# Performance work log

Measured on AMD Instinct MI355X. Metric: run time of the kernel, lower is better.

## Reference

```python
import jax, jax.numpy as jnp
import numpy as np

NUM_CLASSES = 10000
FEAT_DIM = 1024
BATCH = 4096


def setup_inputs() -> dict:
    key = jax.random.key(0)
    k1, k2 = jax.random.split(key)
    feat = jax.random.normal(k1, (BATCH, FEAT_DIM), dtype=jnp.float32)
    centers = jax.random.normal(k2, (NUM_CLASSES, FEAT_DIM), dtype=jnp.float32)
    return {"feat": feat, "centers": centers}


def reference(feat, centers):
    # logits = -0.5 * ||feat_b - center_c||^2, computed via the GEMM rewrite
    # ||a-b||^2 = ||a||^2 + ||b||^2 - 2 a.b  (same math as broadcast-sub-square-sum,
    # but avoids the [B, C, D] intermediate and uses tensor-core matmul).
    feat_sq = jnp.sum(feat * feat, axis=-1, keepdims=True)          # [B, 1]
    cent_sq = jnp.sum(centers * centers, axis=-1)[None, :]          # [1, C]
    cross = jnp.einsum('bd,cd->bc', feat, centers)                  # [B, C]
    dist = feat_sq + cent_sq - 2.0 * cross                          # [B, C]
    logits = -0.5 * dist
    return logits
```

## Files before the change

### kernel.cpp

```cpp
#include <hip/hip_runtime.h>
#include <hip/hip_bf16.h>
#include <stdint.h>

#define M_DIM 4096
#define N_DIM 10000
#define K_DIM 1024
#define GM (M_DIM / 256)
#define GN ((N_DIM + 255) / 256)
#define NT (K_DIM / 32)

typedef __attribute__((ext_vector_type(8))) short bf16x8;
typedef __attribute__((ext_vector_type(4))) float f32x4;

#define BAR()      asm volatile("s_barrier" ::: "memory")
#define WAITVM4()  asm volatile("s_waitcnt vmcnt(4)" ::: "memory")
#define WAITVM0()  asm volatile("s_waitcnt vmcnt(0)" ::: "memory")
#define WAITLGKM() asm volatile("s_waitcnt lgkmcnt(0)" ::: "memory")

__device__ __forceinline__ void async_ld16(const void* g, void* l) {
    __builtin_amdgcn_global_load_lds(
        (const __attribute__((address_space(1))) unsigned int*)g,
        (__attribute__((address_space(3))) unsigned int*)l,
        16, 0, 0);
}

__device__ __forceinline__ unsigned short f2bf(float f) {
    unsigned u = __float_as_uint(f);
    unsigned r = (u + 0x7FFFu + ((u >> 16) & 1u)) >> 16;
    return (unsigned short)r;
}

__global__ __launch_bounds__(256) void prep_rows(
    const float* __restrict__ feat, const float* __restrict__ cent,
    unsigned short* __restrict__ featbf, unsigned short* __restrict__ centbf,
    float* __restrict__ fsq, float* __restrict__ csq)
{
    const int wlane = threadIdx.x & 63;
    const int wid   = blockIdx.x * 4 + (threadIdx.x >> 6);
    const int nw    = gridDim.x * 4;
    for (int row = wid; row < M_DIM + N_DIM; row += nw) {
        const float* in;
        unsigned short* outb;
        float* sqp;
        if (row < M_DIM) {
            in = feat + (size_t)row * K_DIM;
            outb = featbf + (size_t)row * K_DIM;
            sqp = fsq + row;
        } else {
            const int r2 = row - M_DIM;
            in = cent + (size_t)r2 * K_DIM;
            outb = centbf + (size_t)r2 * K_DIM;
            sqp = csq + r2;
        }
        float s = 0.f;
        #pragma unroll
        for (int c = 0; c < 4; c++) {
            float4 v = ((const float4*)in)[wlane + c * 64];
            ushort4 pk;
            pk.x = f2bf(v.x); pk.y = f2bf(v.y); pk.z = f2bf(v.z); pk.w = f2bf(v.w);
            ((ushort4*)outb)[wlane + c * 64] = pk;
            s += v.x * v.x + v.y * v.y + v.z * v.z + v.w * v.w;
        }
        #pragma unroll
        for (int off = 32; off > 0; off >>= 1) s += __shfl_down(s, off, 64);
        if (wlane == 0) *sqp = s;
    }
}

__global__ __launch_bounds__(512, 2) void gemm_bt(
    const unsigned short* __restrict__ A,
    const unsigned short* __restrict__ B,
    const float* __restrict__ fsq, const float* __restrict__ csq,
    float* __restrict__ out)
{
    __shared__ unsigned short smem[49152];

    const int tid  = threadIdx.x;
    const int lane = tid & 63;
    const int wave = tid >> 6;
    const int wm = wave & 1;
    const int wn = wave >> 1;
    const int mlane = lane & 15;
    const int quad  = lane >> 4;
    const int fr  = (mlane >> 1) & 3;
    const int qx  = (quad ^ fr) << 4;

    const int bid = blockIdx.x;
    const int xcd = bid & 7;
    const int idx = bid >> 3;
    const int r0  = xcd * 80 + idx;
    const int bm  = r0 & 15;
    const int bn  = r0 >> 4;

    const int arow_base = bm * 256;
    const int brow_base = bn * 256;

    const unsigned short* gA[2];
    const unsigned short* gB[2];
    int ldsA[2], ldsB[2];
    #pragma unroll
    for (int i = 0; i < 2; i++) {
        const int s   = i * 512 + tid;
        const int row = s >> 2;
        const int sc  = s & 3;
        const int kof = (sc ^ ((row >> 1) & 3)) << 3;
        gA[i] = A + (size_t)(arow_base + row) * K_DIM + kof;
        int br = brow_base + row; if (br > N_DIM - 1) br = N_DIM - 1;
        gB[i] = B + (size_t)br * K_DIM + kof;
        ldsA[i] = s * 16;
        ldsB[i] = 16384 + s * 16;
    }

    #define STAGE_A(t2, nbb)                                                  \
        do {                                                                  \
            async_ld16(gA[0] + (size_t)(t2) * 32, (char*)smem + (nbb) + ldsA[0]); \
            async_ld16(gA[1] + (size_t)(t2) * 32, (char*)smem + (nbb) + ldsA[1]); \
        } while (0)
    #define STAGE_B(t2, nbb)                                                  \
        do {                                                                  \
            async_ld16(gB[0] + (size_t)(t2) * 32, (char*)smem + (nbb) + ldsB[0]); \
            async_ld16(gB[1] + (size_t)(t2) * 32, (char*)smem + (nbb) + ldsB[1]); \
        } while (0)

    f32x4 acc[8][4];
    #pragma unroll
    for (int i = 0; i < 8; i++)
        #pragma unroll
        for (int j = 0; j < 4; j++) {
            f32x4 z = {0.f, 0.f, 0.f, 0.f};
            acc[i][j] = z;
        }

    const int aBase = (wm * 128 + mlane) * 64 + qx;
    const int bBase = 16384 + (wn * 64 + mlane) * 64 + qx;

    STAGE_A(0, 0); STAGE_B(0, 0);
    STAGE_A(1, 32768); STAGE_B(1, 32768);
    WAITVM4();
    BAR();

    int bb = 0;
    for (int t = 0; t < NT; ++t) {
        int nb = bb - 32768; if (nb < 0) nb = 65536;
        const char* base = (const char*)smem + bb;
        bf16x8 af[4], bfv[4];

        #pragma unroll
        for (int i = 0; i < 4; i++) {
            af[i]  = *(const bf16x8*)(base + aBase + i * 1024);
            bfv[i] = *(const bf16x8*)(base + bBase + i * 1024);
        }
        if (t + 2 < NT) STAGE_A(t + 2, nb);
        BAR();
        WAITLGKM();
        __builtin_amdgcn_s_setprio(1);
        #pragma unroll
        for (int i = 0; i < 4; i++)
            #pragma unroll
            for (int j = 0; j < 4; j++)
                acc[i][j] = __builtin_amdgcn_mfma_f32_16x16x32_bf16(
                    af[i], bfv[j], acc[i][j], 0, 0, 0);
        __builtin_amdgcn_s_setprio(0);
        BAR();

        #pragma unroll
        for (int i = 0; i < 4; i++)
            af[i] = *(const bf16x8*)(base + aBase + 4096 + i * 1024);
        if (t + 2 < NT) STAGE_B(t + 2, nb);
        BAR();
        WAITLGKM();
        __builtin_amdgcn_s_setprio(1);
        #pragma unroll
        for (int i = 0; i < 4; i++)
            #pragma unroll
            for (int j = 0; j < 4; j++)
                acc[4 + i][j] = __builtin_amdgcn_mfma_f32_16x16x32_bf16(
                    af[i], bfv[j], acc[4 + i][j], 0, 0, 0);
        __builtin_amdgcn_s_setprio(0);

        if (t < NT - 1) {
            if (t + 2 < NT) { WAITVM4(); } else { WAITVM0(); }
        }
        BAR();

        bb += 32768; if (bb > 65536) bb = 0;
    }
    #undef STAGE_A
    #undef STAGE_B

    float* W = (float*)smem + wave * 1088;
    const int rbase0 = arow_base + wm * 128;
    const int cbase  = brow_base + wn * 64 + mlane;
    const int rb_col4 = mlane * 4;
    const int gcol4  = brow_base + wn * 64 + rb_col4;
    const bool colok = gcol4 < N_DIM;

    #pragma unroll
    for (int i = 0; i < 8; i++) {
        float frow[4];
        #pragma unroll
        for (int r = 0; r < 4; r++)
            frow[r] = -0.5f * fsq[rbase0 + i * 16 + quad * 4 + r];
        #pragma unroll
        for (int j = 0; j < 4; j++) {
            int col = cbase + j * 16;
            float cs = -0.5f * csq[col < N_DIM ? col : (N_DIM - 1)];
            #pragma unroll
            for (int r = 0; r < 4; r++)
                W[(quad * 4 + r) * 68 + j * 16 + mlane] = acc[i][j][r] + frow[r] + cs;
        }
        WAITLGKM();
        #pragma unroll
        for (int s = 0; s < 4; s++) {
            int rl = s * 4 + quad;
            f32x4 v = *(const f32x4*)&W[rl * 68 + rb_col4];
            if (colok) {
                int grow = rbase0 + i * 16 + rl;
                __builtin_nontemporal_store(v, (f32x4*)&out[(size_t)grow * N_DIM + gcol4]);
            }
        }
        WAITLGKM();
    }
}

extern "C" void kernel_launch(void* const* d_in, const int* in_sizes, int n_in,
                              void* d_out, int out_size, void* d_ws, size_t ws_size,
                              hipStream_t stream) {
    const float* feat = (const float*)d_in[0];
    const float* cent = (const float*)d_in[1];
    float* out = (float*)d_out;

    char* ws = (char*)d_ws;
    unsigned short* featbf = (unsigned short*)ws;
    unsigned short* centbf = (unsigned short*)(ws + 8388608);
    float* fsq = (float*)(ws + 8388608 + 20480000);
    float* csq = (float*)(ws + 8388608 + 20480000 + 16384);

    prep_rows<<<1024, 256, 0, stream>>>(feat, cent, featbf, centbf, fsq, csq);

    gemm_bt<<<GM * GN, 512, 0, stream>>>(featbf, centbf, fsq, csq, out);
}
```

Before: 293.1 us.

## Deepen GEMM pipeline to four LDS stages and split K-step into quarter phases

Grows shared memory from three to four 32KB buffers so global-to-LDS prefetch runs three K-tiles ahead instead of two. Each K iteration is split into four phases that each read two A fragments and issue one async load, with a barrier between phases. This aims to hide more global-load latency and interleave loads with MFMA more finely. In exchange it uses 128KB LDS per block, which may cut the number of blocks per CU below the two that launch_bounds requests, and it adds more barriers per iteration.

Result: no change. 295.5 us (+0.8%).

```diff
diff --git a/kernel.cpp b/kernel.cpp
--- a/kernel.cpp
+++ b/kernel.cpp
@@ -13,6 +13,7 @@
 typedef __attribute__((ext_vector_type(4))) float f32x4;
 
 #define BAR()      asm volatile("s_barrier" ::: "memory")
+#define WAITVM8()  asm volatile("s_waitcnt vmcnt(8)" ::: "memory")
 #define WAITVM4()  asm volatile("s_waitcnt vmcnt(4)" ::: "memory")
 #define WAITVM0()  asm volatile("s_waitcnt vmcnt(0)" ::: "memory")
 #define WAITLGKM() asm volatile("s_waitcnt lgkmcnt(0)" ::: "memory")
@@ -73,7 +74,7 @@
     const float* __restrict__ fsq, const float* __restrict__ csq,
     float* __restrict__ out)
 {
-    __shared__ unsigned short smem[49152];
+    __shared__ unsigned short smem[65536];
 
     const int tid  = threadIdx.x;
     const int lane = tid & 63;
@@ -111,82 +112,107 @@
         ldsB[i] = 16384 + s * 16;
     }
 
-    #define STAGE_A(t2, nbb)                                                  \
+    f32x4 acc[8][4];
+    #pragma unroll
+    for (int i = 0; i < 8; i++)
+        #pragma unroll
+        for (int j = 0; j < 4; j++) {
+            f32x4 z = {0.f, 0.f, 0.f, 0.f};
+            acc[i][j] = z;
+        }
+
+    const int aBase = (wm * 128 + mlane) * 64 + qx;
+    const int bBase = 16384 + (wn * 64 + mlane) * 64 + qx;
+
+    #define STAGE_FULL(t2, nbb)                                               \
         do {                                                                  \
             async_ld16(gA[0] + (size_t)(t2) * 32, (char*)smem + (nbb) + ldsA[0]); \
             async_ld16(gA[1] + (size_t)(t2) * 32, (char*)smem + (nbb) + ldsA[1]); \
-        } while (0)
-    #define STAGE_B(t2, nbb)                                                  \
-        do {                                                                  \
             async_ld16(gB[0] + (size_t)(t2) * 32, (char*)smem + (nbb) + ldsB[0]); \
             async_ld16(gB[1] + (size_t)(t2) * 32, (char*)smem + (nbb) + ldsB[1]); \
         } while (0)
-
-    f32x4 acc[8][4];
-    #pragma unroll
-    for (int i = 0; i < 8; i++)
-        #pragma unroll
-        for (int j = 0; j < 4; j++) {
-            f32x4 z = {0.f, 0.f, 0.f, 0.f};
-            acc[i][j] = z;
-        }
-
-    const int aBase = (wm * 128 + mlane) * 64 + qx;
-    const int bBase = 16384 + (wn * 64 + mlane) * 64 + qx;
-
-    STAGE_A(0, 0); STAGE_B(0, 0);
-    STAGE_A(1, 32768); STAGE_B(1, 32768);
-    WAITVM4();
+    STAGE_FULL(0, 0);
+    STAGE_FULL(1, 32768);
+    STAGE_FULL(2, 65536);
+    WAITVM8();
     BAR();
 
-    int bb = 0;
     for (int t = 0; t < NT; ++t) {
-        int nb = bb - 32768; if (nb < 0) nb = 65536;
-        const char* base = (const char*)smem + bb;
-        bf16x8 af[4], bfv[4];
-
-        #pragma unroll
-        for (int i = 0; i < 4; i++) {
-            af[i]  = *(const bf16x8*)(base + aBase + i * 1024);
-            bfv[i] = *(const bf16x8*)(base + bBase + i * 1024);
-        }
-        if (t + 2 < NT) STAGE_A(t + 2, nb);
-        BAR();
-        WAITLGKM();
-        __builtin_amdgcn_s_setprio(1);
-        #pragma unroll
-        for (int i = 0; i < 4; i++)
-            #pragma unroll
-            for (int j = 0; j < 4; j++)
-                acc[i][j] = __builtin_amdgcn_mfma_f32_16x16x32_bf16(
-                    af[i], bfv[j], acc[i][j], 0, 0, 0);
-        __builtin_amdgcn_s_setprio(0);
-        BAR();
-
-        #pragma unroll
-        for (int i = 0; i < 4; i++)
-            af[i] = *(const bf16x8*)(base + aBase + 4096 + i * 1024);
-        if (t + 2 < NT) STAGE_B(t + 2, nb);
-        BAR();
-        WAITLGKM();
-        __builtin_amdgcn_s_setprio(1);
-        #pragma unroll
-        for (int i = 0; i < 4; i++)
-            #pragma unroll
-            for (int j = 0; j < 4; j++)
-                acc[4 + i][j] = __builtin_amdgcn_mfma_f32_16x16x32_bf16(
-                    af[i], bfv[j], acc[4 + i][j], 0, 0, 0);
+        const char* base = (const char*)smem + (t & 3) * 32768;
+        const int  nb    = ((t + 3) & 3) * 32768;
+        const bool st    = (t + 3 < NT);
+        bf16x8 bfv[4], af0, af1;
+
+        #pragma unroll
+        for (int j = 0; j < 4; j++)
+            bfv[j] = *(const bf16x8*)(base + bBase + j * 1024);
+        af0 = *(const bf16x8*)(base + aBase + 0 * 1024);
+        af1 = *(const bf16x8*)(base + aBase + 1 * 1024);
+        if (st) async_ld16(gA[0] + (size_t)(t + 3) * 32, (char*)smem + nb + ldsA[0]);
+        BAR();
+        WAITLGKM();
+        __builtin_amdgcn_s_setprio(1);
+        #pragma unroll
+        for (int j = 0; j < 4; j++)
+            acc[0][j] = __builtin_amdgcn_mfma_f32_16x16x32_bf16(af0, bfv[j], acc[0][j], 0, 0, 0);
+        #pragma unroll
+        for (int j = 0; j < 4; j++)
+            acc[1][j] = __builtin_amdgcn_mfma_f32_16x16x32_bf16(af1, bfv[j], acc[1][j], 0, 0, 0);
+        __builtin_amdgcn_s_setprio(0);
+        BAR();
+
+        af0 = *(const bf16x8*)(base + aBase + 2 * 1024);
+        af1 = *(const bf16x8*)(base + aBase + 3 * 1024);
+        if (st) async_ld16(gA[1] + (size_t)(t + 3) * 32, (char*)smem + nb + ldsA[1]);
+        BAR();
+        WAITLGKM();
+        __builtin_amdgcn_s_setprio(1);
+        #pragma unroll
+        for (int j = 0; j < 4; j++)
+            acc[2][j] = __builtin_amdgcn_mfma_f32_16x16x32_bf16(af0, bfv[j], acc[2][j], 0, 0, 0);
+        #pragma unroll
+        for (int j = 0; j < 4; j++)
+            acc[3][j] = __builtin_amdgcn_mfma_f32_16x16x32_bf16(af1, bfv[j], acc[3][j], 0, 0, 0);
+        __builtin_amdgcn_s_setprio(0);
+        BAR();
+
+        af0 = *(const bf16x8*)(base + aBase + 4 * 1024);
+        af1 = *(const bf16x8*)(base + aBase + 5 * 1024);
+        if (st) async_ld16(gB[0] + (size_t)(t + 3) * 32, (char*)smem + nb + ldsB[0]);
+        BAR();
+        WAITLGKM();
+        __builtin_amdgcn_s_setprio(1);
+        #pragma unroll
+        for (int j = 0; j < 4; j++)
+            acc[4][j] = __builtin_amdgcn_mfma_f32_16x16x32_bf16(af0, bfv[j], acc[4][j], 0, 0, 0);
+        #pragma unroll
+        for (int j = 0; j < 4; j++)
+            acc[5][j] = __builtin_amdgcn_mfma_f32_16x16x32_bf16(af1, bfv[j], acc[5][j], 0, 0, 0);
+        __builtin_amdgcn_s_setprio(0);
+        BAR();
+
+        af0 = *(const bf16x8*)(base + aBase + 6 * 1024);
+        af1 = *(const bf16x8*)(base + aBase + 7 * 1024);
+        if (st) async_ld16(gB[1] + (size_t)(t + 3) * 32, (char*)smem + nb + ldsB[1]);
+        BAR();
+        WAITLGKM();
+        __builtin_amdgcn_s_setprio(1);
+        #pragma unroll
+        for (int j = 0; j < 4; j++)
+            acc[6][j] = __builtin_amdgcn_mfma_f32_16x16x32_bf16(af0, bfv[j], acc[6][j], 0, 0, 0);
+        #pragma unroll
+        for (int j = 0; j < 4; j++)
+            acc[7][j] = __builtin_amdgcn_mfma_f32_16x16x32_bf16(af1, bfv[j], acc[7][j], 0, 0, 0);
         __builtin_amdgcn_s_setprio(0);
 
         if (t < NT - 1) {
-            if (t + 2 < NT) { WAITVM4(); } else { WAITVM0(); }
-        }
-        BAR();
-
-        bb += 32768; if (bb > 65536) bb = 0;
-    }
-    #undef STAGE_A
-    #undef STAGE_B
+            if (t < NT - 3)       { WAITVM8(); }
+            else if (t == NT - 3) { WAITVM4(); }
+            else                  { WAITVM0(); }
+        }
+        BAR();
+    }
+    #undef STAGE_FULL
 
     float* W = (float*)smem + wave * 1088;
     const int rbase0 = arow_base + wm * 128;
```
